# Kernel optimization log

Measured on AMD Instinct MI355X. Metric: run time of the kernel, lower is better.

Reference implementation:

```python
import jax, jax.numpy as jnp
import numpy as np

S, B, D, H = 1024, 64, 1024, 1024


def setup_inputs() -> dict:
    key = jax.random.key(0)
    ks = jax.random.split(key, 18)
    stdv = 1.0 / np.sqrt(H)  # per reset_parameters
    inp = {"Xt": jax.random.normal(ks[0], (S, B, D), dtype=jnp.float32)}
    wnames = ["iiW", "hiW", "ifW", "hfW", "igW", "hgW", "ioW", "hoW"]
    bnames = ["iiB", "hiB", "ifB", "hfB", "igB", "hgB", "ioB", "hoB"]
    for i, n in enumerate(wnames):
        inp[n] = jax.random.uniform(ks[1 + i], (H, D if n[0] == "i" else H),
                                    minval=-stdv, maxval=stdv, dtype=jnp.float32)
    for i, n in enumerate(bnames):
        inp[n] = jax.random.uniform(ks[9 + i], (H,), minval=-stdv, maxval=stdv,
                                    dtype=jnp.float32)
    return inp


def reference(Xt, iiW, hiW, ifW, hfW, igW, hgW, ioW, hoW,
              iiB, hiB, ifB, hfB, igB, hgB, ioB, hoB):
    # single-layer LSTM, batch_first=False: scan over seq dim 0.
    # Math matches torch forward_one: separate input/hidden linears per gate,
    # actF = actC = tanh, dropout = 0.
    bias_i = iiB + hiB  # fuse constant bias sums once
    bias_f = ifB + hfB
    bias_g = igB + hgB
    bias_o = ioB + hoB

    def step(carry, x):
        h, c = carry  # [B, H] each
        I = jax.nn.sigmoid(x @ iiW.T + h @ hiW.T + bias_i)
        F = jax.nn.sigmoid(x @ ifW.T + h @ hfW.T + bias_f)
        G = jnp.tanh(x @ igW.T + h @ hgW.T + bias_g)
        O = jax.nn.sigmoid(x @ ioW.T + h @ hoW.T + bias_o)
        c_ = F * c + I * G
        y = O * jnp.tanh(c_)
        return (y, c_), y

    h0 = jnp.zeros((Xt.shape[1], hiW.shape[0]), dtype=Xt.dtype)
    c0 = jnp.zeros_like(h0)
    (hT, cT), Yt = jax.lax.scan(step, (h0, c0), Xt)
    return Yt, hT, cT  # stack_output=True -> Yt is [S, B, H]
```

## Files before the change

### kernel.cpp

```cpp
#include <hip/hip_runtime.h>
#include <hip/hip_bf16.h>
#include <stdint.h>


typedef __attribute__((ext_vector_type(8))) short bf16x8;
typedef __attribute__((ext_vector_type(4))) float f32x4;

__device__ __forceinline__ unsigned short f2bf(float f) {
    unsigned u = __builtin_bit_cast(unsigned, f);
    return (unsigned short)((u + 0x7fffu + ((u >> 16) & 1u)) >> 16);
}
__device__ __forceinline__ float fast_sigmoid(float x) {
    return __builtin_amdgcn_rcpf(1.f + __expf(-x));
}
__device__ __forceinline__ float fast_tanh(float x) {
    float xc = fminf(fmaxf(x, -9.f), 9.f);
    float e = __expf(2.f * xc);
    return (e - 1.f) * __builtin_amdgcn_rcpf(e + 1.f);
}

__global__ void init_kernel(const float* __restrict__ iiB, const float* __restrict__ hiB,
                            const float* __restrict__ ifB, const float* __restrict__ hfB,
                            const float* __restrict__ igB, const float* __restrict__ hgB,
                            const float* __restrict__ ioB, const float* __restrict__ hoB,
                            float* __restrict__ bias, unsigned short* __restrict__ hbuf0,
                            float* __restrict__ c_ws, unsigned int* __restrict__ bar) {
    int tid = blockIdx.x * 256 + threadIdx.x;
    if (tid < 128) bar[tid] = 0u;
    if (tid < 4096) {
        int g = tid >> 10, j = tid & 1023;
        const float* ib = (g == 0 ? iiB : g == 1 ? ifB : g == 2 ? igB : ioB);
        const float* hb = (g == 0 ? hiB : g == 1 ? hfB : g == 2 ? hgB : hoB);
        bias[tid] = ib[j] + hb[j];
    }
    for (int i = tid; i < 65536; i += 16384) {
        __hip_atomic_store(hbuf0 + i, (unsigned short)0, __ATOMIC_RELAXED, __HIP_MEMORY_SCOPE_AGENT);
        c_ws[i] = 0.f;
    }
}

__global__ void prep_weights(const float* __restrict__ iiW, const float* __restrict__ hiW,
                             const float* __restrict__ ifW, const float* __restrict__ hfW,
                             const float* __restrict__ igW, const float* __restrict__ hgW,
                             const float* __restrict__ ioW, const float* __restrict__ hoW,
                             unsigned short* __restrict__ Wx, unsigned short* __restrict__ Wh) {
    int n = blockIdx.x;
    int g = n >> 10, j = n & 1023;
    const float* wx = (g == 0 ? iiW : g == 1 ? ifW : g == 2 ? igW : ioW) + (size_t)j * 1024;
    const float* wh = (g == 0 ? hiW : g == 1 ? hfW : g == 2 ? hgW : hoW) + (size_t)j * 1024;
    int k = threadIdx.x * 4;
    float4 a = *(const float4*)(wx + k);
    float4 b = *(const float4*)(wh + k);
    ushort4 ra = { f2bf(a.x), f2bf(a.y), f2bf(a.z), f2bf(a.w) };
    ushort4 rb = { f2bf(b.x), f2bf(b.y), f2bf(b.z), f2bf(b.w) };
    *(ushort4*)(Wx + (size_t)n * 1024 + k) = ra;
    *(ushort4*)(Wh + (size_t)n * 1024 + k) = rb;
}

__global__ __launch_bounds__(256, 2) void xproj_gemm(const float* __restrict__ A,
                                                     const unsigned short* __restrict__ Wx,
                                                     const float* __restrict__ bias,
                                                     float* __restrict__ C) {
    __shared__ __align__(16) unsigned short Asm[128 * 32];
    __shared__ __align__(16) unsigned short Bsm[128 * 32];
    int tid = threadIdx.x;
    int lane = tid & 63, wv = tid >> 6;
    int l15 = lane & 15, l4 = lane >> 4;
    int wrow = wv >> 1, wcol = wv & 1;
    int bn0 = blockIdx.x * 128, bm0 = blockIdx.y * 128;
    f32x4 acc[4][4] = {};

    for (int kk = 0; kk < 32; ++kk) {
        int k0 = kk * 32;
        __syncthreads();
#pragma unroll
        for (int it = 0; it < 2; ++it) {
            int tau = it * 256 + tid;
            int row = tau >> 2, slot = tau & 3;
            const float* src = A + (size_t)(bm0 + row) * 1024 + k0 + slot * 8;
            float4 x0 = *(const float4*)src;
            float4 x1 = *(const float4*)(src + 4);
            bf16x8 pk;
            pk[0] = (short)f2bf(x0.x); pk[1] = (short)f2bf(x0.y);
            pk[2] = (short)f2bf(x0.z); pk[3] = (short)f2bf(x0.w);
            pk[4] = (short)f2bf(x1.x); pk[5] = (short)f2bf(x1.y);
            pk[6] = (short)f2bf(x1.z); pk[7] = (short)f2bf(x1.w);
            int dslot = slot ^ (row & 3);
            *(bf16x8*)((char*)Asm + row * 64 + dslot * 16) = pk;
        }
#pragma unroll
        for (int it = 0; it < 2; ++it) {
            int tau = it * 256 + tid;
            int row = tau >> 2, slot = tau & 3;
            int sslot = slot ^ (row & 3);
            const unsigned short* src = Wx + (size_t)(bn0 + row) * 1024 + k0 + sslot * 8;
            char* ldsb = (char*)Bsm + it * 4096 + wv * 1024;
            __builtin_amdgcn_global_load_lds((const __attribute__((address_space(1))) void*)src,
                                             (__attribute__((address_space(3))) void*)ldsb, 16, 0, 0);
        }
        __syncthreads();
        bf16x8 af[4], bfv[4];
#pragma unroll
        for (int i = 0; i < 4; ++i) {
            int rowa = wrow * 64 + i * 16 + l15;
            int sa = l4 ^ (rowa & 3);
            af[i] = *(const bf16x8*)((const char*)Asm + rowa * 64 + sa * 16);
            int rowb = wcol * 64 + i * 16 + l15;
            int sb = l4 ^ (rowb & 3);
            bfv[i] = *(const bf16x8*)((const char*)Bsm + rowb * 64 + sb * 16);
        }
#pragma unroll
        for (int i = 0; i < 4; ++i)
#pragma unroll
            for (int j = 0; j < 4; ++j)
                acc[i][j] = __builtin_amdgcn_mfma_f32_16x16x32_bf16(af[i], bfv[j], acc[i][j], 0, 0, 0);
    }
#pragma unroll
    for (int i = 0; i < 4; ++i) {
        int m = bm0 + wrow * 64 + i * 16 + l4 * 4;
#pragma unroll
        for (int j = 0; j < 4; ++j) {
            int n = bn0 + wcol * 64 + j * 16 + l15;
            int col = (n & 1023) * 4 + (n >> 10);
            float bs = bias[n];
#pragma unroll
            for (int r = 0; r < 4; ++r)
                C[(size_t)(m + r) * 4096 + col] = acc[i][j][r] + bs;
        }
    }
}

__global__ __launch_bounds__(256, 1) void lstm_steps(const float* __restrict__ xproj,
                                                     unsigned short* __restrict__ hbuf,
                                                     float* __restrict__ c_ws,
                                                     const unsigned short* __restrict__ Wh,
                                                     unsigned int* __restrict__ flags,
                                                     float* __restrict__ out,
                                                     int t0, int T) {
    __shared__ float red[8192];
    int tid = threadIdx.x, lane = tid & 63, wv = tid >> 6;
    int l15 = lane & 15, l4 = lane >> 4;
    int wg = blockIdx.x;
    int mhalf = wg & 1;
    int cg = wg >> 1;
    int j0 = cg * 16;
    unsigned int* myflags = flags + mhalf * 64;
    const unsigned int* pollp = myflags + wv * 16 + l15;

    bf16x8 w[8][4];
#pragma unroll
    for (int ks = 0; ks < 8; ++ks)
#pragma unroll
        for (int g = 0; g < 4; ++g) {
            int n = g * 1024 + j0 + l15;
            int k = wv * 256 + ks * 32 + l4 * 8;
            w[ks][g] = *(const bf16x8*)(Wh + (size_t)n * 1024 + k);
        }
#pragma unroll
    for (int ks = 0; ks < 8; ++ks)
#pragma unroll
        for (int g = 0; g < 4; ++g)
            asm volatile("" : "+a"(w[ks][g]));

    float c_reg[2];
    int bq[2];
#pragma unroll
    for (int pi = 0; pi < 2; ++pi) {
        int p = wv * 2 + pi, m = p >> 2, r = p & 3;
        bq[pi] = mhalf * 32 + m * 16 + l4 * 4 + r;
        c_reg[pi] = c_ws[(size_t)bq[pi] * 1024 + j0 + l15];
    }

    float4 xp_cur[2], xp_nxt[2];
#pragma unroll
    for (int pi = 0; pi < 2; ++pi)
        xp_cur[pi] = *(const float4*)(xproj + (size_t)bq[pi] * 4096 + (j0 + l15) * 4);

    float yv[2] = {0.f, 0.f};

    for (int tl = 0; tl < T; ++tl) {
        int ts = t0 + tl;
        int par = ts & 1;
        const unsigned short* hb = hbuf + (size_t)par * 65536;

        if (tl > 0) {
#pragma unroll
            for (int pi = 0; pi < 2; ++pi)
                out[(size_t)((ts - 1) * 64 + bq[pi]) * 1024 + j0 + l15] = yv[pi];
        }
        int tln = (tl + 1 < T) ? tl + 1 : tl;
#pragma unroll
        for (int pi = 0; pi < 2; ++pi)
            xp_nxt[pi] = *(const float4*)(xproj + (size_t)(tln * 64 + bq[pi]) * 4096 + (j0 + l15) * 4);

        {
            unsigned tgt = (unsigned)ts;
            for (;;) {
                unsigned f = __hip_atomic_load(pollp, __ATOMIC_RELAXED, __HIP_MEMORY_SCOPE_AGENT);
                if (__ballot(f >= tgt) == ~0ull) break;
                __builtin_amdgcn_s_sleep(1);
            }
        }

        bf16x8 af[2][8];
#pragma unroll
        for (int m = 0; m < 2; ++m) {
            int row = mhalf * 32 + m * 16 + l15;
            const unsigned short* rp = hb + (size_t)row * 1024 + wv * 256 + l4 * 8;
#pragma unroll
            for (int ks = 0; ks < 8; ++ks) {
                unsigned long long* p = (unsigned long long*)(rp + ks * 32);
                union { unsigned long long q[2]; bf16x8 v; } u;
                u.q[0] = __hip_atomic_load(p,     __ATOMIC_RELAXED, __HIP_MEMORY_SCOPE_AGENT);
                u.q[1] = __hip_atomic_load(p + 1, __ATOMIC_RELAXED, __HIP_MEMORY_SCOPE_AGENT);
                af[m][ks] = u.v;
            }
        }

        f32x4 acc[2][4] = {};
#pragma unroll
        for (int ks = 0; ks < 8; ++ks)
#pragma unroll
            for (int m = 0; m < 2; ++m)
#pragma unroll
                for (int g = 0; g < 4; ++g)
                    acc[m][g] = __builtin_amdgcn_mfma_f32_16x16x32_bf16(af[m][ks], w[ks][g], acc[m][g], 0, 0, 0);

#pragma unroll
        for (int m = 0; m < 2; ++m)
#pragma unroll
            for (int g = 0; g < 4; ++g)
#pragma unroll
                for (int r = 0; r < 4; ++r)
                    red[(wv * 32 + m * 16 + g * 4 + r) * 64 + lane] = acc[m][g][r];
        __syncthreads();

#pragma unroll
        for (int pi = 0; pi < 2; ++pi) {
            int p = wv * 2 + pi, m = p >> 2, r = p & 3;
            int b = bq[pi];
            int j = j0 + l15;
            const float* xpf = (const float*)&xp_cur[pi];
            float pre[4];
#pragma unroll
            for (int g = 0; g < 4; ++g) {
                int s = m * 16 + g * 4 + r;
                pre[g] = red[s * 64 + lane] + red[(32 + s) * 64 + lane] +
                         red[(64 + s) * 64 + lane] + red[(96 + s) * 64 + lane] + xpf[g];
            }
            float I = fast_sigmoid(pre[0]);
            float F = fast_sigmoid(pre[1]);
            float G = fast_tanh(pre[2]);
            float O = fast_sigmoid(pre[3]);
            float c = F * c_reg[pi] + I * G;
            c_reg[pi] = c;
            float y = O * fast_tanh(c);
            yv[pi] = y;
            __hip_atomic_store(hbuf + (size_t)(par ^ 1) * 65536 + (size_t)b * 1024 + j,
                               f2bf(y), __ATOMIC_RELAXED, __HIP_MEMORY_SCOPE_AGENT);
        }

        __syncthreads();
        if (tid == 0)
            __hip_atomic_store(myflags + cg, (unsigned)(ts + 1),
                               __ATOMIC_RELAXED, __HIP_MEMORY_SCOPE_AGENT);

        xp_cur[0] = xp_nxt[0];
        xp_cur[1] = xp_nxt[1];
    }
#pragma unroll
    for (int pi = 0; pi < 2; ++pi) {
        int b = bq[pi];
        int j = j0 + l15;
        out[(size_t)((t0 + T - 1) * 64 + b) * 1024 + j] = yv[pi];
        if (t0 + T == 1024) {
            out[67108864u + (size_t)b * 1024 + j] = yv[pi];
            out[67108864u + 65536u + (size_t)b * 1024 + j] = c_reg[pi];
        }
        c_ws[(size_t)b * 1024 + j0 + l15] = c_reg[pi];
    }
}

extern "C" void kernel_launch(void* const* d_in, const int* in_sizes, int n_in,
                              void* d_out, int out_size, void* d_ws, size_t ws_size,
                              hipStream_t stream) {
    (void)in_sizes; (void)n_in; (void)out_size;
    const float* Xt = (const float*)d_in[0];
    const float* W[8]; for (int i = 0; i < 8; ++i) W[i] = (const float*)d_in[1 + i];
    const float* Bv[8]; for (int i = 0; i < 8; ++i) Bv[i] = (const float*)d_in[9 + i];
    float* out = (float*)d_out;
    uint8_t* ws = (uint8_t*)d_ws;

    unsigned int*  bar   = (unsigned int*)(ws + 0);
    float*         bias  = (float*)(ws + 512);
    unsigned short* hbuf = (unsigned short*)(ws + 16896);
    float*         c_ws  = (float*)(ws + 279040);
    unsigned short* Wx   = (unsigned short*)(ws + 541184);
    unsigned short* Wh   = (unsigned short*)(ws + 8929792);
    float*         xproj = (float*)(ws + 17318400);

    size_t avail = ws_size > 17318400 ? ws_size - 17318400 : 0;
    int T = 4;
    for (int t = 1024; t >= 4; t >>= 1)
        if ((size_t)t * 1048576ull <= avail) { T = t; break; }

    init_kernel<<<64, 256, 0, stream>>>(Bv[0], Bv[1], Bv[2], Bv[3], Bv[4], Bv[5], Bv[6], Bv[7],
                                        bias, hbuf, c_ws, bar);
    prep_weights<<<4096, 256, 0, stream>>>(W[0], W[1], W[2], W[3], W[4], W[5], W[6], W[7], Wx, Wh);

    int nch = 1024 / T;
    for (int c = 0; c < nch; ++c) {
        xproj_gemm<<<dim3(32, T / 2), 256, 0, stream>>>(Xt + (size_t)c * T * 65536, Wx, bias, xproj);
        lstm_steps<<<128, 256, 0, stream>>>(xproj, hbuf, c_ws, Wh, bar, out, c * T, T);
    }
}
```

Baseline: 7.266 ms.

## Replace per-block flag barrier with timestep-tagged hidden-state words

Each hidden-state element is now stored as a 32-bit word holding the bf16 value in its low half and a timestep tag in its high half. Consumers spin directly on the data they need until every tag matches, and the per-workgroup flag array and the extra syncthreads-then-flag handoff are dropped. This is meant to cut the step-to-step synchronisation latency by removing a separate flag round-trip. In exchange, hidden-state traffic doubles, each poll re-reads the full operand tile, the xproj prefetch is removed, and outputs are now written inside the step.

```diff
diff --git a/kernel.cpp b/kernel.cpp
--- a/kernel.cpp
+++ b/kernel.cpp
@@ -23,10 +23,9 @@
                             const float* __restrict__ ifB, const float* __restrict__ hfB,
                             const float* __restrict__ igB, const float* __restrict__ hgB,
                             const float* __restrict__ ioB, const float* __restrict__ hoB,
-                            float* __restrict__ bias, unsigned short* __restrict__ hbuf0,
-                            float* __restrict__ c_ws, unsigned int* __restrict__ bar) {
+                            float* __restrict__ bias, unsigned int* __restrict__ hbuf,
+                            float* __restrict__ c_ws) {
     int tid = blockIdx.x * 256 + threadIdx.x;
-    if (tid < 128) bar[tid] = 0u;
     if (tid < 4096) {
         int g = tid >> 10, j = tid & 1023;
         const float* ib = (g == 0 ? iiB : g == 1 ? ifB : g == 2 ? igB : ioB);
@@ -34,7 +33,8 @@
         bias[tid] = ib[j] + hb[j];
     }
     for (int i = tid; i < 65536; i += 16384) {
-        __hip_atomic_store(hbuf0 + i, (unsigned short)0, __ATOMIC_RELAXED, __HIP_MEMORY_SCOPE_AGENT);
+        hbuf[i]         = 0u;
+        hbuf[65536 + i] = 0xFFFF0000u;
         c_ws[i] = 0.f;
     }
 }
@@ -131,10 +131,9 @@
 }
 
 __global__ __launch_bounds__(256, 1) void lstm_steps(const float* __restrict__ xproj,
-                                                     unsigned short* __restrict__ hbuf,
+                                                     unsigned int* __restrict__ hbuf,
                                                      float* __restrict__ c_ws,
                                                      const unsigned short* __restrict__ Wh,
-                                                     unsigned int* __restrict__ flags,
                                                      float* __restrict__ out,
                                                      int t0, int T) {
     __shared__ float red[8192];
@@ -144,8 +143,6 @@
     int mhalf = wg & 1;
     int cg = wg >> 1;
     int j0 = cg * 16;
-    unsigned int* myflags = flags + mhalf * 64;
-    const unsigned int* pollp = myflags + wv * 16 + l15;
 
     bf16x8 w[8][4];
 #pragma unroll
@@ -171,51 +168,56 @@
         c_reg[pi] = c_ws[(size_t)bq[pi] * 1024 + j0 + l15];
     }
 
-    float4 xp_cur[2], xp_nxt[2];
-#pragma unroll
-    for (int pi = 0; pi < 2; ++pi)
-        xp_cur[pi] = *(const float4*)(xproj + (size_t)bq[pi] * 4096 + (j0 + l15) * 4);
-
     float yv[2] = {0.f, 0.f};
 
     for (int tl = 0; tl < T; ++tl) {
         int ts = t0 + tl;
         int par = ts & 1;
-        const unsigned short* hb = hbuf + (size_t)par * 65536;
-
-        if (tl > 0) {
-#pragma unroll
-            for (int pi = 0; pi < 2; ++pi)
-                out[(size_t)((ts - 1) * 64 + bq[pi]) * 1024 + j0 + l15] = yv[pi];
-        }
-        int tln = (tl + 1 < T) ? tl + 1 : tl;
+        const unsigned long long* hb64 =
+            (const unsigned long long*)(hbuf + (size_t)par * 65536);
+
+        float4 xp[2];
 #pragma unroll
         for (int pi = 0; pi < 2; ++pi)
-            xp_nxt[pi] = *(const float4*)(xproj + (size_t)(tln * 64 + bq[pi]) * 4096 + (j0 + l15) * 4);
-
+            xp[pi] = *(const float4*)(xproj + (size_t)(tl * 64 + bq[pi]) * 4096 + (j0 + l15) * 4);
+
+        unsigned long long raw[2][8][4];
         {
-            unsigned tgt = (unsigned)ts;
+            unsigned tg = (unsigned)ts;
             for (;;) {
-                unsigned f = __hip_atomic_load(pollp, __ATOMIC_RELAXED, __HIP_MEMORY_SCOPE_AGENT);
-                if (__ballot(f >= tgt) == ~0ull) break;
+                bool ok = true;
+#pragma unroll
+                for (int m = 0; m < 2; ++m) {
+                    size_t rb = ((size_t)(mhalf * 32 + m * 16 + l15) * 1024 + wv * 256 + l4 * 8) >> 1;
+#pragma unroll
+                    for (int ks = 0; ks < 8; ++ks) {
+#pragma unroll
+                        for (int q = 0; q < 4; ++q) {
+                            unsigned long long r = __hip_atomic_load(
+                                hb64 + rb + ks * 16 + q, __ATOMIC_RELAXED, __HIP_MEMORY_SCOPE_AGENT);
+                            raw[m][ks][q] = r;
+                            ok &= (((unsigned)(r >> 16) & 0xFFFFu) == tg) &
+                                  ((unsigned)(r >> 48) == tg);
+                        }
+                    }
+                }
+                if (__ballot(ok) == ~0ull) break;
                 __builtin_amdgcn_s_sleep(1);
             }
         }
-
         bf16x8 af[2][8];
 #pragma unroll
-        for (int m = 0; m < 2; ++m) {
-            int row = mhalf * 32 + m * 16 + l15;
-            const unsigned short* rp = hb + (size_t)row * 1024 + wv * 256 + l4 * 8;
+        for (int m = 0; m < 2; ++m)
 #pragma unroll
             for (int ks = 0; ks < 8; ++ks) {
-                unsigned long long* p = (unsigned long long*)(rp + ks * 32);
-                union { unsigned long long q[2]; bf16x8 v; } u;
-                u.q[0] = __hip_atomic_load(p,     __ATOMIC_RELAXED, __HIP_MEMORY_SCOPE_AGENT);
-                u.q[1] = __hip_atomic_load(p + 1, __ATOMIC_RELAXED, __HIP_MEMORY_SCOPE_AGENT);
-                af[m][ks] = u.v;
+                union { unsigned u[4]; bf16x8 v; } t;
+#pragma unroll
+                for (int q = 0; q < 4; ++q) {
+                    unsigned long long r = raw[m][ks][q];
+                    t.u[q] = ((unsigned)r & 0xFFFFu) | (((unsigned)(r >> 32) & 0xFFFFu) << 16);
+                }
+                af[m][ks] = t.v;
             }
-        }
 
         f32x4 acc[2][4] = {};
 #pragma unroll
@@ -235,12 +237,14 @@
                     red[(wv * 32 + m * 16 + g * 4 + r) * 64 + lane] = acc[m][g][r];
         __syncthreads();
 
+        unsigned ntag = (unsigned)(ts + 1) << 16;
+        unsigned int* hbn = hbuf + (size_t)(par ^ 1) * 65536;
 #pragma unroll
         for (int pi = 0; pi < 2; ++pi) {
             int p = wv * 2 + pi, m = p >> 2, r = p & 3;
             int b = bq[pi];
             int j = j0 + l15;
-            const float* xpf = (const float*)&xp_cur[pi];
+            const float* xpf = (const float*)&xp[pi];
             float pre[4];
 #pragma unroll
             for (int g = 0; g < 4; ++g) {
@@ -256,23 +260,16 @@
             c_reg[pi] = c;
             float y = O * fast_tanh(c);
             yv[pi] = y;
-            __hip_atomic_store(hbuf + (size_t)(par ^ 1) * 65536 + (size_t)b * 1024 + j,
-                               f2bf(y), __ATOMIC_RELAXED, __HIP_MEMORY_SCOPE_AGENT);
-        }
-
+            __hip_atomic_store(hbn + (size_t)b * 1024 + j, ntag | (unsigned)f2bf(y),
+                               __ATOMIC_RELAXED, __HIP_MEMORY_SCOPE_AGENT);
+            out[(size_t)(ts * 64 + b) * 1024 + j] = y;
+        }
         __syncthreads();
-        if (tid == 0)
-            __hip_atomic_store(myflags + cg, (unsigned)(ts + 1),
-                               __ATOMIC_RELAXED, __HIP_MEMORY_SCOPE_AGENT);
-
-        xp_cur[0] = xp_nxt[0];
-        xp_cur[1] = xp_nxt[1];
     }
 #pragma unroll
     for (int pi = 0; pi < 2; ++pi) {
         int b = bq[pi];
         int j = j0 + l15;
-        out[(size_t)((t0 + T - 1) * 64 + b) * 1024 + j] = yv[pi];
         if (t0 + T == 1024) {
             out[67108864u + (size_t)b * 1024 + j] = yv[pi];
             out[67108864u + 65536u + (size_t)b * 1024 + j] = c_reg[pi];
@@ -291,26 +288,25 @@
     float* out = (float*)d_out;
     uint8_t* ws = (uint8_t*)d_ws;
 
-    unsigned int*  bar   = (unsigned int*)(ws + 0);
-    float*         bias  = (float*)(ws + 512);
-    unsigned short* hbuf = (unsigned short*)(ws + 16896);
-    float*         c_ws  = (float*)(ws + 279040);
-    unsigned short* Wx   = (unsigned short*)(ws + 541184);
-    unsigned short* Wh   = (unsigned short*)(ws + 8929792);
-    float*         xproj = (float*)(ws + 17318400);
-
-    size_t avail = ws_size > 17318400 ? ws_size - 17318400 : 0;
+    float*          bias  = (float*)(ws + 512);
+    unsigned int*   hbuf  = (unsigned int*)(ws + 16896);
+    float*          c_ws  = (float*)(ws + 541184);
+    unsigned short* Wx    = (unsigned short*)(ws + 803328);
+    unsigned short* Wh    = (unsigned short*)(ws + 9191936);
+    float*          xproj = (float*)(ws + 17580544);
+
+    size_t avail = ws_size > 17580544 ? ws_size - 17580544 : 0;
     int T = 4;
     for (int t = 1024; t >= 4; t >>= 1)
         if ((size_t)t * 1048576ull <= avail) { T = t; break; }
 
     init_kernel<<<64, 256, 0, stream>>>(Bv[0], Bv[1], Bv[2], Bv[3], Bv[4], Bv[5], Bv[6], Bv[7],
-                                        bias, hbuf, c_ws, bar);
+                                        bias, hbuf, c_ws);
     prep_weights<<<4096, 256, 0, stream>>>(W[0], W[1], W[2], W[3], W[4], W[5], W[6], W[7], Wx, Wh);
 
     int nch = 1024 / T;
     for (int c = 0; c < nch; ++c) {
         xproj_gemm<<<dim3(32, T / 2), 256, 0, stream>>>(Xt + (size_t)c * T * 65536, Wx, bias, xproj);
-        lstm_steps<<<128, 256, 0, stream>>>(xproj, hbuf, c_ws, Wh, bar, out, c * T, T);
-    }
-}
+        lstm_steps<<<128, 256, 0, stream>>>(xproj, hbuf, c_ws, Wh, out, c * T, T);
+    }
+}
```

Measured after the change: 13.82 ms. 1.9x slower.
